# Performance work log

Measured on AMD Instinct MI355X. Metric: run time of the kernel, lower is better.

The kernel has to match this reference:

```python
import jax, jax.numpy as jnp
import numpy as np

B, S, D, H = 2, 2048, 1024, 16
Dh = D // H
EPS = 1e-6


def _layernorm(x, alpha, beta):
    # torch.std is unbiased (ddof=1); module divides by (std + eps)
    m = jnp.mean(x, axis=-1, keepdims=True)
    var = jnp.sum((x - m) ** 2, axis=-1, keepdims=True) / (x.shape[-1] - 1)
    return alpha * (x - m) / (jnp.sqrt(var) + EPS) + beta


def setup_inputs() -> dict:
    key = jax.random.key(0)
    ks = jax.random.split(key, 12)
    sc = 0.02
    return {
        "x": jax.random.normal(ks[0], (B, S, D), jnp.float32),
        "src_mask": jnp.ones((B, 1, S), jnp.int32),
        # per-head q/k/v projections stacked over heads: [H, D, Dh]
        "Wq": jax.random.normal(ks[1], (H, D, Dh), jnp.float32) * sc,
        "bq": jnp.zeros((H, Dh), jnp.float32),
        "Wk": jax.random.normal(ks[2], (H, D, Dh), jnp.float32) * sc,
        "bk": jnp.zeros((H, Dh), jnp.float32),
        "Wv": jax.random.normal(ks[3], (H, D, Dh), jnp.float32) * sc,
        "bv": jnp.zeros((H, Dh), jnp.float32),
        # FFN: D -> 4D -> D
        "W1": jax.random.normal(ks[4], (D, 4 * D), jnp.float32) * sc,
        "b1": jnp.zeros((4 * D,), jnp.float32),
        "W2": jax.random.normal(ks[5], (4 * D, D), jnp.float32) * sc,
        "b2": jnp.zeros((D,), jnp.float32),
        # two LayerNorms (residual connections)
        "alpha1": jnp.ones((D,), jnp.float32),
        "beta1": jnp.zeros((D,), jnp.float32),
        "alpha2": jnp.ones((D,), jnp.float32),
        "beta2": jnp.zeros((D,), jnp.float32),
    }


def _encoder_block(x, src_mask, Wq, bq, Wk, bk, Wv, bv, W1, b1, W2, b2,
                   alpha1, beta1, alpha2, beta2):
    # --- multi-head self-attention (all heads vectorized) ---
    q = jnp.einsum('bsd,hde->bhse', x, Wq) + bq[None, :, None, :]
    k = jnp.einsum('bsd,hde->bhse', x, Wk) + bk[None, :, None, :]
    v = jnp.einsum('bsd,hde->bhse', x, Wv) + bv[None, :, None, :]
    wei = jnp.einsum('bhse,bhte->bhst', q, k) * (Dh ** -0.5)  # [B,H,S,S]
    wei = jnp.where(src_mask[:, None, :, :] == 0, -jnp.inf, wei)
    wei = jax.nn.softmax(wei, axis=-1)
    attn = jnp.einsum('bhst,bhte->bhse', wei, v)  # [B,H,S,Dh]
    attn = attn.transpose(0, 2, 1, 3).reshape(x.shape[0], x.shape[1], D)
    # NOTE: original module never applies its output projection (self.pro unused)
    # residual 1: x + norm(sublayer(x))
    x = x + _layernorm(attn, alpha1, beta1)
    # --- feed-forward ---
    h = jax.nn.relu(x @ W1 + b1)
    ffn = h @ W2 + b2
    x = x + _layernorm(ffn, alpha2, beta2)
    return x


def reference(x, src_mask, Wq, bq, Wk, bk, Wv, bv, W1, b1, W2, b2,
              alpha1, beta1, alpha2, beta2):
    return _encoder_block(x, src_mask, Wq, bq, Wk, bk, Wv, bv,
                          W1, b1, W2, b2, alpha1, beta1, alpha2, beta2)
```

## Files before the change

### kernel.cpp

```cpp
#include <hip/hip_runtime.h>


#define DEV __device__ __forceinline__

typedef unsigned short u16;
typedef unsigned int u32;
typedef __attribute__((ext_vector_type(8))) short bfrag;
typedef __attribute__((ext_vector_type(8))) __bf16 bf16x8;
typedef __attribute__((ext_vector_type(2))) __bf16 bf16x2_t;
typedef __attribute__((ext_vector_type(4))) unsigned int u32x4;
typedef __attribute__((ext_vector_type(4))) float facc;
typedef __attribute__((ext_vector_type(16))) float facc16;

DEV float bf2f(u16 u) {
  unsigned int x = ((unsigned int)u) << 16;
  return __builtin_bit_cast(float, x);
}
DEV u16 f2bf(float f) {
  unsigned int x = __builtin_bit_cast(unsigned int, f);
  x += 0x7fffu + ((x >> 16) & 1u);
  return (u16)(x >> 16);
}

DEV void gl2lds16(const u16* g, u16* l) {
  auto gp = (const __attribute__((address_space(1))) unsigned int*)(g);
  auto lp = (__attribute__((address_space(3))) unsigned int*)(l);
  __builtin_amdgcn_global_load_lds(gp, lp, 16, 0, 0);
}

DEV facc mfma16(bfrag a, bfrag b, facc c) {
  return __builtin_amdgcn_mfma_f32_16x16x32_bf16(
      __builtin_bit_cast(bf16x8, a), __builtin_bit_cast(bf16x8, b), c, 0, 0, 0);
}

DEV facc16 mfma32(bfrag a, bfrag b, facc16 c) {
  return __builtin_amdgcn_mfma_f32_32x32x16_bf16(
      __builtin_bit_cast(bf16x8, a), __builtin_bit_cast(bf16x8, b), c, 0, 0, 0);
}

DEV u32 pk2(float a, float b) {
  bf16x2_t v;
  v[0] = (__bf16)a;
  v[1] = (__bf16)b;
  return __builtin_bit_cast(u32, v);
}

DEV void pswap(u32& a, u32& b) {
  asm volatile("v_permlane32_swap_b32 %0, %1" : "+v"(a), "+v"(b));
}

__global__ __launch_bounds__(256) void prep_kernel(
    const float* __restrict__ Wq, const float* __restrict__ Wk,
    const float* __restrict__ Wv, u16* __restrict__ WqkvT,
    const float* __restrict__ W1, u16* __restrict__ W1T,
    const float* __restrict__ W2, u16* __restrict__ W2T,
    const float* __restrict__ x, u16* __restrict__ xb) {
  __shared__ float tile[32][33];
  const int job = blockIdx.x;
  const int tr = threadIdx.x >> 5, tc = threadIdx.x & 31;

  if (job >= 11264) {
    const int i = (job - 11264) * 1024 + threadIdx.x * 4;
    const float4 v = *(const float4*)(x + i);
    ushort4 o;
    o.x = f2bf(v.x); o.y = f2bf(v.y); o.z = f2bf(v.z); o.w = f2bf(v.w);
    *(ushort4*)(xb + i) = o;
    return;
  }

  const float* in;
  u16* out;
  int C, R, c0, r0;
  if (job < 3072) {
    const int z = job >> 6, rem = job & 63;
    const int which = z >> 4, h = z & 15;
    in = ((which == 0) ? Wq : (which == 1) ? Wk : Wv) + (size_t)h * 1024 * 64;
    out = WqkvT + ((size_t)which * 1024 + h * 64) * 1024;
    C = 64; R = 1024;
    c0 = (rem & 1) * 32; r0 = (rem >> 1) * 32;
  } else if (job < 7168) {
    const int rem = job - 3072;
    in = W1; out = W1T; C = 4096; R = 1024;
    c0 = (rem & 127) * 32; r0 = (rem >> 7) * 32;
  } else {
    const int rem = job - 7168;
    in = W2; out = W2T; C = 1024; R = 4096;
    c0 = (rem & 31) * 32; r0 = (rem >> 5) * 32;
  }
#pragma unroll
  for (int k = 0; k < 4; k++)
    tile[tr + 8 * k][tc] = in[(size_t)(r0 + tr + 8 * k) * C + c0 + tc];
  __syncthreads();
#pragma unroll
  for (int k = 0; k < 4; k++)
    out[(size_t)(c0 + tr + 8 * k) * R + r0 + tc] = f2bf(tile[tc][tr + 8 * k]);
}

template <int MODE>
__global__ __launch_bounds__(512, 2) void gemm256(
    const u16* __restrict__ A, int lda, const u16* __restrict__ Bt, int ldb,
    int M, int N, int K,
    const float* __restrict__ bias0, const float* __restrict__ bias1,
    const float* __restrict__ bias2,
    void* __restrict__ out0, void* __restrict__ out1, void* __restrict__ out2) {
  __shared__ __align__(16) u16 As[2][256 * 64];
  __shared__ __align__(16) u16 Bs[2][256 * 64];
  const int tid = threadIdx.x;
  const int lane = tid & 63;
  const int wave = tid >> 6;
  const int laneM = lane & 15, quad = lane >> 4;
  const int kx = laneM & 7;
  const int m0 = blockIdx.x * 256, n0 = blockIdx.y * 256;
  const int wm = wave & 1, wn = wave >> 1;

  const u16* Ab = A;
  const u16* Bb = Bt;
  if (MODE == 3) {
    Ab += (size_t)blockIdx.z * K;
    Bb += (size_t)blockIdx.z * K;
  }

  int srow[4], skl[4];
#pragma unroll
  for (int c = 0; c < 4; c++) {
    const int slot = wave * 256 + c * 64 + lane;
    srow[c] = slot >> 3;
    skl[c] = ((slot & 7) ^ (srow[c] & 7)) * 8;
  }

  auto stage = [&](int X, int t) {
    const u16* Asrc = Ab + (size_t)t * 64;
    const u16* Bsrc = Bb + (size_t)t * 64;
#pragma unroll
    for (int c = 0; c < 4; c++)
      gl2lds16(Asrc + (size_t)(m0 + srow[c]) * lda + skl[c],
               As[X] + (size_t)(wave * 256 + c * 64) * 8);
#pragma unroll
    for (int c = 0; c < 4; c++)
      gl2lds16(Bsrc + (size_t)(n0 + srow[c]) * ldb + skl[c],
               Bs[X] + (size_t)(wave * 256 + c * 64) * 8);
  };

  facc acc[8][4] = {};

  const int NT = K >> 6;
  stage(0, 0);

  for (int t = 0; t < NT; ++t) {
    const int cur = t & 1;
    if (t + 1 < NT) {
      stage(cur ^ 1, t + 1);
      asm volatile("s_waitcnt vmcnt(8)" ::: "memory");
    } else {
      asm volatile("s_waitcnt vmcnt(0)" ::: "memory");
    }
    __builtin_amdgcn_s_barrier();

    const u16* as = As[cur];
    const u16* bs = Bs[cur];
#pragma unroll
    for (int k32 = 0; k32 < 2; ++k32) {
      bfrag af[8], bf[4];
#pragma unroll
      for (int i = 0; i < 8; i++) {
        const int row = wm * 128 + i * 16 + laneM;
        af[i] = *(const bfrag*)(as + row * 64 + (((k32 * 4 + quad) ^ kx) * 8));
      }
#pragma unroll
      for (int j = 0; j < 4; j++) {
        const int row = wn * 64 + j * 16 + laneM;
        bf[j] = *(const bfrag*)(bs + row * 64 + (((k32 * 4 + quad) ^ kx) * 8));
      }
#pragma unroll
      for (int i = 0; i < 8; i++)
#pragma unroll
        for (int j = 0; j < 4; j++)
          acc[i][j] = mfma16(af[i], bf[j], acc[i][j]);
    }
    __builtin_amdgcn_s_barrier();
  }

#pragma unroll
  for (int i = 0; i < 8; i++) {
#pragma unroll
    for (int j = 0; j < 4; j++) {
      const int col = n0 + wn * 64 + j * 16 + laneM;
      const int row0 = m0 + wm * 128 + i * 16 + quad * 4;
      if (MODE == 0) {
        const int which = col >> 10, c = col & 1023;
        const float* bp = (which == 0) ? bias0 : (which == 1) ? bias1 : bias2;
        u16* op = (u16*)((which == 0) ? out0 : (which == 1) ? out1 : out2);
        const float bb = bp[c];
        const int b = row0 >> 11, s0 = row0 & 2047;
        const int h = c >> 6, e = c & 63;
        if (which == 2) {
          ushort4 pk;
          pk.x = f2bf(acc[i][j][0] + bb);
          pk.y = f2bf(acc[i][j][1] + bb);
          pk.z = f2bf(acc[i][j][2] + bb);
          pk.w = f2bf(acc[i][j][3] + bb);
          *(ushort4*)(op + ((size_t)((b * 16 + h) * 64 + e)) * 2048 + s0) = pk;
        } else {
#pragma unroll
          for (int v = 0; v < 4; v++)
            op[((size_t)(b * 16 + h) * 2048 + s0 + v) * 64 + e] =
                f2bf(acc[i][j][v] + bb);
        }
      } else if (MODE == 1) {
        const float bb = bias0[col];
#pragma unroll
        for (int v = 0; v < 4; v++)
          ((u16*)out0)[(size_t)(row0 + v) * N + col] =
              f2bf(fmaxf(acc[i][j][v] + bb, 0.0f));
      } else {
        const int z = blockIdx.z;
        u16* op = (u16*)((z < 2) ? out0 : out1) + (size_t)(z & 1) * M * N;
#pragma unroll
        for (int v = 0; v < 4; v++)
          op[(size_t)(row0 + v) * N + col] = f2bf(acc[i][j][v]);
      }
    }
  }
}

__global__ __launch_bounds__(256) void attn_kernel(
    const u16* __restrict__ Qb, const u16* __restrict__ Kb,
    const u16* __restrict__ VTg, const int* __restrict__ mask,
    u16* __restrict__ Opart, float* __restrict__ lbuf) {
  __shared__ __align__(16) u16 KT[2][64 * 64];
  __shared__ __align__(16) u16 VS[2][64 * 64];
  __shared__ float MB[1024];
  const int tid = threadIdx.x;
  const int lane = tid & 63;
  const int wave = tid >> 6;
  const int col = lane & 31, hi = lane >> 5;
  const int bh = blockIdx.x, b = bh >> 4, h = bh & 15;
  const int q0 = blockIdx.y * 128;
  const int z = blockIdx.z;
  const int sbase = z * 1024;
  const u16* Qh = Qb + (size_t)bh * 2048 * 64;
  const u16* Kh = Kb + (size_t)bh * 2048 * 64 + (size_t)sbase * 64;
  const u16* Vh = VTg + (size_t)bh * 64 * 2048 + sbase;
  const float SC = 0.125f * 1.4426950408889634f;

  const int q = q0 + wave * 32 + col;
  bfrag qf[4];
#pragma unroll
  for (int ds = 0; ds < 4; ds++)
    qf[ds] = *(const bfrag*)(Qh + (size_t)q * 64 + ds * 16 + 8 * hi);

#pragma unroll
  for (int t = 0; t < 4; t++) {
    const int i = t * 256 + tid;
    MB[i] = mask[b * 2048 + sbase + i] ? 0.0f : -1e30f;
  }

  const int s0 = wave * 128;
  const int sA = s0 + lane, sB = s0 + 64 + lane;
  const int rA = sA & 63, cA = sA >> 6;
  const int rB = sB & 63, cB = sB >> 6;

  gl2lds16(Kh + (size_t)rA * 64 + cA * 8, KT[0] + (size_t)s0 * 8);
  gl2lds16(Kh + (size_t)rB * 64 + cB * 8, KT[0] + (size_t)(s0 + 64) * 8);
  gl2lds16(Vh + (size_t)rA * 2048 + cA * 8, VS[0] + (size_t)s0 * 8);
  gl2lds16(Vh + (size_t)rB * 2048 + cB * 8, VS[0] + (size_t)(s0 + 64) * 8);
  __syncthreads();

  float lsum = 0.0f;
  facc16 oacc0 = (facc16)0.0f, oacc1 = (facc16)0.0f;
  const int hb = hi * 512;
  const int c8 = col * 8;

  for (int it = 0; it < 16; ++it) {
    const int t0 = it * 64;
    const int cur = it & 1;
    if (it < 15) {
      const int nxt = cur ^ 1;
      const int t0n = t0 + 64;
      gl2lds16(Kh + (size_t)(t0n + rA) * 64 + cA * 8, KT[nxt] + (size_t)s0 * 8);
      gl2lds16(Kh + (size_t)(t0n + rB) * 64 + cB * 8,
               KT[nxt] + (size_t)(s0 + 64) * 8);
      gl2lds16(Vh + (size_t)rA * 2048 + t0n + cA * 8, VS[nxt] + (size_t)s0 * 8);
      gl2lds16(Vh + (size_t)rB * 2048 + t0n + cB * 8,
               VS[nxt] + (size_t)(s0 + 64) * 8);
      asm volatile("s_waitcnt vmcnt(4)" ::: "memory");
    } else {
      asm volatile("s_waitcnt vmcnt(0)" ::: "memory");
    }
    __builtin_amdgcn_s_barrier();

    const u16* kb = KT[cur];
    const u16* vb = VS[cur];
#pragma unroll
    for (int tile = 0; tile < 2; tile++) {
      facc16 sacc = (facc16)0.0f;
#pragma unroll
      for (int ds = 0; ds < 4; ds++) {
        bfrag kf = *(const bfrag*)(kb + ds * 1024 + hb + tile * 256 + c8);
        sacc = mfma32(kf, qf[ds], sacc);
      }
      u32 w[8];
#pragma unroll
      for (int g = 0; g < 4; g++) {
        const float4 mg = *(const float4*)(MB + t0 + tile * 32 + g * 8 + 4 * hi);
        const float p0 = __builtin_amdgcn_exp2f(fmaf(sacc[g * 4 + 0], SC, mg.x));
        const float p1 = __builtin_amdgcn_exp2f(fmaf(sacc[g * 4 + 1], SC, mg.y));
        const float p2 = __builtin_amdgcn_exp2f(fmaf(sacc[g * 4 + 2], SC, mg.z));
        const float p3 = __builtin_amdgcn_exp2f(fmaf(sacc[g * 4 + 3], SC, mg.w));
        lsum += (p0 + p1) + (p2 + p3);
        w[g * 2 + 0] = pk2(p0, p1);
        w[g * 2 + 1] = pk2(p2, p3);
      }
      pswap(w[0], w[2]);
      pswap(w[1], w[3]);
      pswap(w[4], w[6]);
      pswap(w[5], w[7]);
#pragma unroll
      for (int sub = 0; sub < 2; sub++) {
        u32x4 pv4;
        pv4[0] = w[sub * 4 + 0];
        pv4[1] = w[sub * 4 + 1];
        pv4[2] = w[sub * 4 + 2];
        pv4[3] = w[sub * 4 + 3];
        const bfrag pa = __builtin_bit_cast(bfrag, pv4);
        const int ks = tile * 2 + sub;
        {
          bfrag vf = *(const bfrag*)(vb + ks * 1024 + hb + c8);
          oacc0 = mfma32(vf, pa, oacc0);
        }
        {
          bfrag vf = *(const bfrag*)(vb + ks * 1024 + hb + 256 + c8);
          oacc1 = mfma32(vf, pa, oacc1);
        }
      }
    }
    __builtin_amdgcn_s_barrier();
  }

  const float l = lsum + __shfl_xor(lsum, 32, 64);
  if (hi == 0) lbuf[((size_t)(z * 32 + bh)) * 2048 + q] = l;

  u16* dst = Opart + (size_t)z * 4096 * 1024 +
             ((size_t)(b * 2048 + q)) * 1024 + h * 64;
#pragma unroll
  for (int eh = 0; eh < 2; eh++) {
    const facc16& oa = eh ? oacc1 : oacc0;
#pragma unroll
    for (int g = 0; g < 4; g++) {
      ushort4 pk;
      pk.x = f2bf(oa[g * 4 + 0]);
      pk.y = f2bf(oa[g * 4 + 1]);
      pk.z = f2bf(oa[g * 4 + 2]);
      pk.w = f2bf(oa[g * 4 + 3]);
      *(ushort4*)(dst + eh * 32 + g * 8 + 4 * hi) = pk;
    }
  }
}

__global__ __launch_bounds__(256) void ln_attn(
    const float* __restrict__ base, const u16* __restrict__ Opart,
    const float* __restrict__ lbuf,
    const float* __restrict__ alpha, const float* __restrict__ beta,
    float* __restrict__ outf, u16* __restrict__ outb) {
  __shared__ float red[4];
  const int row = blockIdx.x;
  const int t = threadIdx.x;
  const int b = row >> 11, s = row & 2047;
  const int h = t >> 4;
  const size_t off = (size_t)row * 1024 + t * 4;
  const size_t zstride = (size_t)4096 * 1024;

  const float l0 = lbuf[((size_t)(b * 16 + h)) * 2048 + s];
  const float l1 = lbuf[((size_t)(32 + b * 16 + h)) * 2048 + s];
  const float inv = 1.0f / (l0 + l1);

  const ushort4 o0 = *(const ushort4*)(Opart + off);
  const ushort4 o1 = *(const ushort4*)(Opart + zstride + off);
  float4 yv;
  yv.x = (bf2f(o0.x) + bf2f(o1.x)) * inv;
  yv.y = (bf2f(o0.y) + bf2f(o1.y)) * inv;
  yv.z = (bf2f(o0.z) + bf2f(o1.z)) * inv;
  yv.w = (bf2f(o0.w) + bf2f(o1.w)) * inv;

  float sm = yv.x + yv.y + yv.z + yv.w;
#pragma unroll
  for (int o = 1; o < 64; o <<= 1) sm += __shfl_xor(sm, o, 64);
  if ((t & 63) == 0) red[t >> 6] = sm;
  __syncthreads();
  const float mean = (red[0] + red[1] + red[2] + red[3]) * (1.0f / 1024.0f);
  __syncthreads();

  const float d0 = yv.x - mean, d1 = yv.y - mean, d2 = yv.z - mean, d3 = yv.w - mean;
  float ss = d0 * d0 + d1 * d1 + d2 * d2 + d3 * d3;
#pragma unroll
  for (int o = 1; o < 64; o <<= 1) ss += __shfl_xor(ss, o, 64);
  if ((t & 63) == 0) red[t >> 6] = ss;
  __syncthreads();
  const float var = (red[0] + red[1] + red[2] + red[3]) * (1.0f / 1023.0f);
  const float rstd = 1.0f / (sqrtf(var) + 1e-6f);

  const float4 bv = *(const float4*)(base + off);
  const float4 av = *(const float4*)(alpha + (size_t)t * 4);
  const float4 ev = *(const float4*)(beta + (size_t)t * 4);

  float4 ov;
  ov.x = bv.x + av.x * d0 * rstd + ev.x;
  ov.y = bv.y + av.y * d1 * rstd + ev.y;
  ov.z = bv.z + av.z * d2 * rstd + ev.z;
  ov.w = bv.w + av.w * d3 * rstd + ev.w;
  *(float4*)(outf + off) = ov;
  ushort4 ob;
  ob.x = f2bf(ov.x); ob.y = f2bf(ov.y); ob.z = f2bf(ov.z); ob.w = f2bf(ov.w);
  *(ushort4*)(outb + off) = ob;
}

__global__ __launch_bounds__(256) void ln_res2(
    const float* __restrict__ base, const u16* __restrict__ parts0,
    const u16* __restrict__ parts1, const float* __restrict__ biasv,
    const float* __restrict__ alpha, const float* __restrict__ beta,
    float* __restrict__ outf) {
  __shared__ float red[4];
  const int row = blockIdx.x;
  const int t = threadIdx.x;
  const size_t off = (size_t)row * 1024 + t * 4;
  const size_t stride = (size_t)4096 * 1024;

  float4 yv = *(const float4*)(biasv + (size_t)t * 4);
#pragma unroll
  for (int zi = 0; zi < 2; zi++) {
    const ushort4 pz = *(const ushort4*)(parts0 + zi * stride + off);
    yv.x += bf2f(pz.x); yv.y += bf2f(pz.y);
    yv.z += bf2f(pz.z); yv.w += bf2f(pz.w);
  }
#pragma unroll
  for (int zi = 0; zi < 2; zi++) {
    const ushort4 pz = *(const ushort4*)(parts1 + zi * stride + off);
    yv.x += bf2f(pz.x); yv.y += bf2f(pz.y);
    yv.z += bf2f(pz.z); yv.w += bf2f(pz.w);
  }

  float s = yv.x + yv.y + yv.z + yv.w;
#pragma unroll
  for (int o = 1; o < 64; o <<= 1) s += __shfl_xor(s, o, 64);
  if ((t & 63) == 0) red[t >> 6] = s;
  __syncthreads();
  const float mean = (red[0] + red[1] + red[2] + red[3]) * (1.0f / 1024.0f);
  __syncthreads();

  const float d0 = yv.x - mean, d1 = yv.y - mean, d2 = yv.z - mean, d3 = yv.w - mean;
  float ss = d0 * d0 + d1 * d1 + d2 * d2 + d3 * d3;
#pragma unroll
  for (int o = 1; o < 64; o <<= 1) ss += __shfl_xor(ss, o, 64);
  if ((t & 63) == 0) red[t >> 6] = ss;
  __syncthreads();
  const float var = (red[0] + red[1] + red[2] + red[3]) * (1.0f / 1023.0f);
  const float rstd = 1.0f / (sqrtf(var) + 1e-6f);

  const float4 bv = *(const float4*)(base + off);
  const float4 av = *(const float4*)(alpha + (size_t)t * 4);
  const float4 ev = *(const float4*)(beta + (size_t)t * 4);

  float4 ov;
  ov.x = bv.x + av.x * d0 * rstd + ev.x;
  ov.y = bv.y + av.y * d1 * rstd + ev.y;
  ov.z = bv.z + av.z * d2 * rstd + ev.z;
  ov.w = bv.w + av.w * d3 * rstd + ev.w;
  *(float4*)(outf + off) = ov;
}

extern "C" void kernel_launch(void* const* d_in, const int* in_sizes, int n_in,
                              void* d_out, int out_size, void* d_ws,
                              size_t ws_size, hipStream_t stream) {
  const float* x  = (const float*)d_in[0];
  const int* mask = (const int*)d_in[1];
  const float* Wq = (const float*)d_in[2];
  const float* bq = (const float*)d_in[3];
  const float* Wk = (const float*)d_in[4];
  const float* bk = (const float*)d_in[5];
  const float* Wv = (const float*)d_in[6];
  const float* bv = (const float*)d_in[7];
  const float* W1 = (const float*)d_in[8];
  const float* b1 = (const float*)d_in[9];
  const float* W2 = (const float*)d_in[10];
  const float* b2 = (const float*)d_in[11];
  const float* alpha1 = (const float*)d_in[12];
  const float* beta1  = (const float*)d_in[13];
  const float* alpha2 = (const float*)d_in[14];
  const float* beta2  = (const float*)d_in[15];
  float* out = (float*)d_out;

  char* p = (char*)d_ws;
  u16* xb      = (u16*)p;  p += (size_t)4096 * 1024 * 2;
  u16* WqkvT   = (u16*)p;  p += (size_t)3072 * 1024 * 2;
  u16* W1T     = (u16*)p;  p += (size_t)4096 * 1024 * 2;
  u16* W2T     = (u16*)p;  p += (size_t)1024 * 4096 * 2;
  u16* Qbuf    = (u16*)p;  p += (size_t)32 * 2048 * 64 * 2;
  u16* Kbuf    = (u16*)p;  p += (size_t)32 * 2048 * 64 * 2;
  u16* Vbuf    = (u16*)p;  p += (size_t)32 * 2048 * 64 * 2;
  u16* attnp   = (u16*)p;  p += (size_t)2 * 4096 * 1024 * 2;
  float* lbuf  = (float*)p; p += (size_t)2 * 32 * 2048 * 4;
  float* x1f   = (float*)p; p += (size_t)4096 * 1024 * 4;
  u16* x1b     = (u16*)p;  p += (size_t)4096 * 1024 * 2;
  u16* hbuf    = (u16*)p;  p += (size_t)4096 * 4096 * 2;
  u16* ffnp    = (u16*)p;  p += (size_t)2 * 4096 * 1024 * 2;

  prep_kernel<<<15360, 256, 0, stream>>>(Wq, Wk, Wv, WqkvT, W1, W1T, W2, W2T,
                                         x, xb);

  gemm256<0><<<dim3(16, 12), 512, 0, stream>>>(
      xb, 1024, WqkvT, 1024, 4096, 3072, 1024, bq, bk, bv, Qbuf, Kbuf, Vbuf);

  attn_kernel<<<dim3(32, 16, 2), 256, 0, stream>>>(Qbuf, Kbuf, Vbuf, mask,
                                                   attnp, lbuf);

  ln_attn<<<4096, 256, 0, stream>>>(x, attnp, lbuf, alpha1, beta1, x1f, x1b);

  gemm256<1><<<dim3(16, 16), 512, 0, stream>>>(
      x1b, 1024, W1T, 1024, 4096, 4096, 1024, b1, nullptr, nullptr,
      hbuf, nullptr, nullptr);

  gemm256<3><<<dim3(16, 4, 4), 512, 0, stream>>>(
      hbuf, 4096, W2T, 4096, 4096, 1024, 1024, nullptr, nullptr, nullptr,
      ffnp, attnp, nullptr);

  ln_res2<<<4096, 256, 0, stream>>>(x1f, ffnp, attnp, b2, alpha2, beta2, out);
}
```

Baseline: 316.7 us.

## Load K/V fragments directly from global memory in attention, drop LDS staging

The attention kernel no longer double-buffers K and V tiles in shared memory via gl2lds with barriers. Each lane now reads its MFMA operand fragments straight from global memory (relying on L1/L2 reuse across the four waves), and the per-iteration barriers are removed. Launch bounds add a minimum-blocks hint of 6 for higher occupancy. This trades LDS traffic and synchronisation for redundant global/cache loads with less latency hiding, since nothing prefetches the next tile any more.

```diff
diff --git a/kernel.cpp b/kernel.cpp
--- a/kernel.cpp
+++ b/kernel.cpp
@@ -223,12 +223,10 @@
   }
 }
 
-__global__ __launch_bounds__(256) void attn_kernel(
+__global__ __launch_bounds__(256, 6) void attn_kernel(
     const u16* __restrict__ Qb, const u16* __restrict__ Kb,
     const u16* __restrict__ VTg, const int* __restrict__ mask,
     u16* __restrict__ Opart, float* __restrict__ lbuf) {
-  __shared__ __align__(16) u16 KT[2][64 * 64];
-  __shared__ __align__(16) u16 VS[2][64 * 64];
   __shared__ float MB[1024];
   const int tid = threadIdx.x;
   const int lane = tid & 63;
@@ -254,49 +252,23 @@
     const int i = t * 256 + tid;
     MB[i] = mask[b * 2048 + sbase + i] ? 0.0f : -1e30f;
   }
-
-  const int s0 = wave * 128;
-  const int sA = s0 + lane, sB = s0 + 64 + lane;
-  const int rA = sA & 63, cA = sA >> 6;
-  const int rB = sB & 63, cB = sB >> 6;
-
-  gl2lds16(Kh + (size_t)rA * 64 + cA * 8, KT[0] + (size_t)s0 * 8);
-  gl2lds16(Kh + (size_t)rB * 64 + cB * 8, KT[0] + (size_t)(s0 + 64) * 8);
-  gl2lds16(Vh + (size_t)rA * 2048 + cA * 8, VS[0] + (size_t)s0 * 8);
-  gl2lds16(Vh + (size_t)rB * 2048 + cB * 8, VS[0] + (size_t)(s0 + 64) * 8);
   __syncthreads();
 
   float lsum = 0.0f;
   facc16 oacc0 = (facc16)0.0f, oacc1 = (facc16)0.0f;
-  const int hb = hi * 512;
-  const int c8 = col * 8;
+
+  const u16* kb0 = Kh + (size_t)col * 64 + 8 * hi;
+  const u16* vb0 = Vh + (size_t)col * 2048 + 8 * hi;
 
   for (int it = 0; it < 16; ++it) {
     const int t0 = it * 64;
-    const int cur = it & 1;
-    if (it < 15) {
-      const int nxt = cur ^ 1;
-      const int t0n = t0 + 64;
-      gl2lds16(Kh + (size_t)(t0n + rA) * 64 + cA * 8, KT[nxt] + (size_t)s0 * 8);
-      gl2lds16(Kh + (size_t)(t0n + rB) * 64 + cB * 8,
-               KT[nxt] + (size_t)(s0 + 64) * 8);
-      gl2lds16(Vh + (size_t)rA * 2048 + t0n + cA * 8, VS[nxt] + (size_t)s0 * 8);
-      gl2lds16(Vh + (size_t)rB * 2048 + t0n + cB * 8,
-               VS[nxt] + (size_t)(s0 + 64) * 8);
-      asm volatile("s_waitcnt vmcnt(4)" ::: "memory");
-    } else {
-      asm volatile("s_waitcnt vmcnt(0)" ::: "memory");
-    }
-    __builtin_amdgcn_s_barrier();
-
-    const u16* kb = KT[cur];
-    const u16* vb = VS[cur];
 #pragma unroll
     for (int tile = 0; tile < 2; tile++) {
+      const u16* kbase = kb0 + (size_t)(t0 + tile * 32) * 64;
       facc16 sacc = (facc16)0.0f;
 #pragma unroll
       for (int ds = 0; ds < 4; ds++) {
-        bfrag kf = *(const bfrag*)(kb + ds * 1024 + hb + tile * 256 + c8);
+        bfrag kf = *(const bfrag*)(kbase + ds * 16);
         sacc = mfma32(kf, qf[ds], sacc);
       }
       u32 w[8];
@@ -323,18 +295,17 @@
         pv4[2] = w[sub * 4 + 2];
         pv4[3] = w[sub * 4 + 3];
         const bfrag pa = __builtin_bit_cast(bfrag, pv4);
-        const int ks = tile * 2 + sub;
+        const u16* vbase = vb0 + t0 + (tile * 2 + sub) * 16;
         {
-          bfrag vf = *(const bfrag*)(vb + ks * 1024 + hb + c8);
+          bfrag vf = *(const bfrag*)(vbase);
           oacc0 = mfma32(vf, pa, oacc0);
         }
         {
-          bfrag vf = *(const bfrag*)(vb + ks * 1024 + hb + 256 + c8);
+          bfrag vf = *(const bfrag*)(vbase + (size_t)32 * 2048);
           oacc1 = mfma32(vf, pa, oacc1);
         }
       }
     }
-    __builtin_amdgcn_s_barrier();
   }
 
   const float l = lsum + __shfl_xor(lsum, 32, 64);
```

After: 425.1 us. 34.2% more time.
